# Performance work log

Hardware: AMD Instinct MI355X
Metric: run time of the kernel (lower is better)

The kernel has to match this reference:

```python
import jax, jax.numpy as jnp
import numpy as np

N, SEQ, HID, ENC, E = 16384, 512, 1024, 256, 8


def setup_inputs() -> dict:
    key = jax.random.key(0)
    ks = jax.random.split(key, 8)
    def w(k, shape, fan_in):
        return jax.random.normal(k, shape, dtype=jnp.float32) * (1.0 / np.sqrt(fan_in))
    return {
        "x": jax.random.normal(ks[0], (N, SEQ), dtype=jnp.float32),
        "ids": jax.random.randint(ks[1], (N,), 0, E),
        "W1": w(ks[2], (SEQ, HID), SEQ),
        "b1": jnp.zeros((HID,), jnp.float32),
        "W2": w(ks[3], (HID, ENC), HID),
        "b2": jnp.zeros((ENC,), jnp.float32),
        "W3": w(ks[4], (E, ENC, HID), ENC),
        "b3": jnp.zeros((E, HID), jnp.float32),
        "W4": w(ks[5], (E, HID, SEQ), HID),
        "b4": jnp.zeros((E, SEQ), jnp.float32),
    }


def reference(x, ids, W1, b1, W2, b2, W3, b3, W4, b4):
    # fixed trunk (shared across all combination IDs)
    h = jax.nn.relu(x @ W1 + b1)          # [N, HID]
    z = jax.nn.relu(h @ W2 + b2)          # [N, ENC]
    # per-combination expert head: Linear(enc,hid)+ReLU+Linear(hid,seq)
    n_experts = W3.shape[0]
    oh = jax.nn.one_hot(ids, n_experts, dtype=x.dtype)  # [N, E] row->expert mask
    y = jnp.zeros((x.shape[0], W4.shape[-1]), dtype=x.dtype)
    for e in range(n_experts):  # small fixed expert count; each iter is a big GEMM
        u = jax.nn.relu(z @ W3[e] + b3[e])             # [N, HID]
        y = y + (u @ W4[e] + b4[e]) * oh[:, e:e + 1]   # scatter-back via mask
    return y
```

## Files before the change

kernel.cpp:

```cpp
#include <hip/hip_runtime.h>
#include <hip/hip_bf16.h>

#define NROWS 16384
#define SEQD  512
#define HIDD  1024
#define ENCD  256
#define NEXP  8
#define NBLK  64
#define MAXTILES 136
#define MPAD_MAX (MAXTILES * 128)

using bf16 = __hip_bfloat16;
typedef __bf16 bf16x8 __attribute__((ext_vector_type(8)));
typedef float  f32x4  __attribute__((ext_vector_type(4)));

enum : size_t {
  OFF_XB   = 0,
  OFF_W1T  = OFF_XB  + (size_t)NROWS * SEQD * 2,
  OFF_W2T  = OFF_W1T + (size_t)HIDD * SEQD * 2,
  OFF_H    = OFF_W2T + (size_t)ENCD * HIDD * 2,
  OFF_W3T  = OFF_H   + (size_t)NROWS * HIDD * 2,
  OFF_W4T  = OFF_W3T + (size_t)NEXP * HIDD * ENCD * 2,
  OFF_Z    = OFF_W4T + (size_t)NEXP * SEQD * HIDD * 2,
  OFF_PERM = OFF_Z   + (size_t)NROWS * ENCD * 2,
  OFF_META = OFF_PERM + (size_t)MPAD_MAX * 4,
  OFF_U    = 0,
  WS_NEED  = OFF_META + 8192
};

__device__ __forceinline__ void gload_lds16(const void* g, void* l) {
  __builtin_amdgcn_global_load_lds(
      (const __attribute__((address_space(1))) void*)g,
      (__attribute__((address_space(3))) void*)l, 16, 0, 0);
}

__global__ void prep_k(const float* __restrict__ x,
                       const float* __restrict__ W1, const float* __restrict__ W2,
                       const float* __restrict__ W3, const float* __restrict__ W4,
                       bf16* __restrict__ Xb, bf16* __restrict__ W1t,
                       bf16* __restrict__ W2t, bf16* __restrict__ W3t,
                       bf16* __restrict__ W4t) {
  __shared__ float t[32][33];
  int b = blockIdx.x;
  const int tid = threadIdx.x;
  if (b < 4096) {
    size_t i = (size_t)b * 256 + tid;
    float4 a = ((const float4*)x)[i * 2];
    float4 c = ((const float4*)x)[i * 2 + 1];
    __align__(16) bf16 v[8] = {
      __float2bfloat16(a.x), __float2bfloat16(a.y), __float2bfloat16(a.z), __float2bfloat16(a.w),
      __float2bfloat16(c.x), __float2bfloat16(c.y), __float2bfloat16(c.z), __float2bfloat16(c.w)};
    *(int4*)(Xb + i * 8) = *(const int4*)v;
    return;
  }
  b -= 4096;
  const float* s; bf16* d; int R, C;
  if (b < 512)              { s = W1; d = W1t; R = SEQD; C = HIDD; }
  else if ((b -= 512) < 256){ s = W2; d = W2t; R = HIDD; C = ENCD; }
  else if ((b -= 256) < 2048){
    int z = b >> 8; b &= 255; s = W3 + (size_t)z * ENCD * HIDD; d = W3t + (size_t)z * ENCD * HIDD;
    R = ENCD; C = HIDD;
  } else {
    b -= 2048; int z = b >> 9; b &= 511;
    s = W4 + (size_t)z * HIDD * SEQD; d = W4t + (size_t)z * HIDD * SEQD;
    R = HIDD; C = SEQD;
  }
  const int nbx = C >> 5;
  const int bx = (b % nbx) * 32, by = (b / nbx) * 32;
  const int tx = tid & 31, ty = tid >> 5;
  #pragma unroll
  for (int i = 0; i < 32; i += 8) t[ty + i][tx] = s[(size_t)(by + ty + i) * C + bx + tx];
  __syncthreads();
  #pragma unroll
  for (int i = 0; i < 32; i += 8)
    d[(size_t)(bx + ty + i) * R + by + tx] = __float2bfloat16(t[tx][ty + i]);
}


__global__ void count_k(const int* __restrict__ ids, int* __restrict__ gh) {
  __shared__ int c[NEXP];
  const int tid = threadIdx.x;
  if (tid < NEXP) c[tid] = 0;
  __syncthreads();
  atomicAdd(&c[ids[blockIdx.x * 256 + tid]], 1);
  __syncthreads();
  if (tid < NEXP) gh[blockIdx.x * NEXP + tid] = c[tid];
}

__global__ __launch_bounds__(1024) void bases_k(int* __restrict__ meta,
                                                int* __restrict__ perm) {
  int* gh        = meta;
  int* bases     = meta + 512;
  int* blockbase = meta + 528;
  __shared__ int counts[NEXP];
  __shared__ int base_s[NEXP + 1];
  const int tid = threadIdx.x;
  if (tid < NEXP) {
    int s = 0;
    for (int b = 0; b < NBLK; ++b) s += gh[b * NEXP + tid];
    counts[tid] = s;
  }
  __syncthreads();
  if (tid == 0) {
    int t = 0;
    for (int e = 0; e < NEXP; ++e) { base_s[e] = t; t += (counts[e] + 127) & ~127; }
    base_s[NEXP] = t;
  }
  __syncthreads();
  if (tid < NEXP) {
    int run = base_s[tid];
    for (int b = 0; b < NBLK; ++b) { blockbase[b * NEXP + tid] = run; run += gh[b * NEXP + tid]; }
  }
  if (tid == 0)
    for (int e = 0; e <= NEXP; ++e) bases[e] = base_s[e];
  #pragma unroll
  for (int e = 0; e < NEXP; ++e) {
    int lo = base_s[e] + counts[e];
    int i  = lo + tid;
    if (i < base_s[e + 1]) perm[i] = -1;
  }
}

__global__ void scatter_k(const int* __restrict__ ids, const int* __restrict__ blockbase,
                          int* __restrict__ perm) {
  __shared__ int wavehist[4][NEXP];
  const int tid = threadIdx.x, w = tid >> 6, lane = tid & 63;
  const int n = blockIdx.x * 256 + tid;
  const int e = ids[n];
  const unsigned long long lt = (1ull << lane) - 1ull;
  int myrank = 0;
  #pragma unroll
  for (int ee = 0; ee < NEXP; ++ee) {
    unsigned long long bb = __ballot(e == ee);
    if (ee == e) myrank = __popcll(bb & lt);
    if (lane == 0) wavehist[w][ee] = __popcll(bb);
  }
  __syncthreads();
  int pre = 0;
  for (int w2 = 0; w2 < w; ++w2) pre += wavehist[w2][e];
  perm[blockbase[blockIdx.x * NEXP + e] + pre + myrank] = n;
}

template <bool GATHER_A, bool EXPERT, bool RELU, bool SCATTER_F32>
__global__ __launch_bounds__(256, 2) void gemm128(
    const bf16* __restrict__ A, const bf16* __restrict__ Bt,
    const float* __restrict__ bias, void* __restrict__ Out,
    int Ncols, int K, const int* __restrict__ perm, const int* __restrict__ bases) {
  __shared__ char lds[65536];

  const int tid  = threadIdx.x;
  const int wid  = tid >> 6;
  const int lane = tid & 63;
  const int lm = lane & 15, l4 = lane >> 4;
  const int wm = wid >> 1, wn = wid & 1;

  const int tileM = blockIdx.x, tileN = blockIdx.y;
  int expert = 0;
  if (EXPERT) {
    const int total = bases[8];
    if (tileM * 128 >= total) return;
    const int r0 = tileM * 128;
    #pragma unroll
    for (int e = 1; e < NEXP; ++e) expert += (r0 >= bases[e]) ? 1 : 0;
    Bt   += (size_t)expert * Ncols * K;
    bias += expert * Ncols;
  }
  const int row0 = tileM * 128, col0 = tileN * 128;

  const bf16* gA[4];
  const bf16* gB[4];
  #pragma unroll
  for (int i = 0; i < 4; ++i) {
    int flat = (i * 4 + wid) * 1024 + lane * 16;
    int r    = flat >> 7;
    int cb   = (flat & 127) ^ ((r & 7) << 4);
    int arow;
    if (GATHER_A) {
      int p = perm[row0 + r];
      arow = (p < 0) ? 0 : p;
    } else {
      arow = row0 + r;
    }
    gA[i] = A  + (size_t)arow * K + (cb >> 1);
    gB[i] = Bt + (size_t)(col0 + r) * K + (cb >> 1);
  }

  f32x4 acc[4][4];
  #pragma unroll
  for (int i = 0; i < 4; ++i)
    #pragma unroll
    for (int j = 0; j < 4; ++j) { f32x4 z = {0.f, 0.f, 0.f, 0.f}; acc[i][j] = z; }

  int aoff[4], boff[4];
  const int swz = (lm & 7) << 4;
  #pragma unroll
  for (int i = 0; i < 4; ++i) {
    int ar = wm * 64 + i * 16 + lm;
    aoff[i] = ar * 128 + ((l4 * 16) ^ swz);
    int br = wn * 64 + i * 16 + lm;
    boff[i] = br * 128 + ((l4 * 16) ^ swz);
  }

  const int nk = K >> 6;
  const int ldsoff = (wid * 4) * 1024 + (lane & 3) * 16 + ((lane >> 2) << 8);
  asm volatile("s_waitcnt vmcnt(0)" ::: "memory");
  __builtin_amdgcn_sched_barrier(0);

  #pragma unroll
  for (int i = 0; i < 4; ++i) {
    gload_lds16(gA[i], lds + (i * 4 + wid) * 1024);
    gload_lds16(gB[i], lds + 16384 + (i * 4 + wid) * 1024);
  }
  #pragma unroll
  for (int i = 0; i < 4; ++i) {
    gload_lds16(gA[i] + 64, lds + 32768 + (i * 4 + wid) * 1024);
    gload_lds16(gB[i] + 64, lds + 32768 + 16384 + (i * 4 + wid) * 1024);
  }

  for (int kt = 0; kt < nk; ++kt) {
    if (kt < nk - 1) asm volatile("s_waitcnt vmcnt(8)" ::: "memory");
    else             asm volatile("s_waitcnt vmcnt(0)" ::: "memory");
    asm volatile("s_barrier" ::: "memory");
    __builtin_amdgcn_sched_barrier(0);

    const char* Ac = lds + (kt & 1) * 32768;
    const char* Bc = Ac + 16384;
    #pragma unroll
    for (int kk = 0; kk < 2; ++kk) {
      bf16x8 af[4], bfr[4];
      #pragma unroll
      for (int i = 0; i < 4; ++i) af[i]  = *(const bf16x8*)(Ac + (aoff[i] ^ (kk * 64)));
      #pragma unroll
      for (int i = 0; i < 4; ++i) bfr[i] = *(const bf16x8*)(Bc + (boff[i] ^ (kk * 64)));
      #pragma unroll
      for (int mi = 0; mi < 4; ++mi)
        #pragma unroll
        for (int ni = 0; ni < 4; ++ni)
          acc[mi][ni] = __builtin_amdgcn_mfma_f32_16x16x32_bf16(af[mi], bfr[ni], acc[mi][ni], 0, 0, 0);
    }

    asm volatile("s_barrier" ::: "memory");
    __builtin_amdgcn_sched_barrier(0);
    if (kt + 2 < nk) {
      char* An = lds + (kt & 1) * 32768;
      #pragma unroll
      for (int i = 0; i < 4; ++i) {
        gload_lds16(gA[i] + (size_t)(kt + 2) * 64, An + (i * 4 + wid) * 1024);
        gload_lds16(gB[i] + (size_t)(kt + 2) * 64, An + 16384 + (i * 4 + wid) * 1024);
      }
    }
  }
  (void)ldsoff;

  float bv[4];
  #pragma unroll
  for (int ni = 0; ni < 4; ++ni) bv[ni] = bias[col0 + wn * 64 + ni * 16 + lm];
  #pragma unroll
  for (int mi = 0; mi < 4; ++mi) {
    #pragma unroll
    for (int r = 0; r < 4; ++r) {
      int rowp = row0 + wm * 64 + mi * 16 + l4 * 4 + r;
      int orow = rowp;
      bool valid = true;
      if (SCATTER_F32) {
        int p = perm[rowp];
        valid = (p >= 0);
        orow  = valid ? p : 0;
      }
      #pragma unroll
      for (int ni = 0; ni < 4; ++ni) {
        float v = acc[mi][ni][r] + bv[ni];
        if (RELU) v = v > 0.f ? v : 0.f;
        int n = col0 + wn * 64 + ni * 16 + lm;
        if (SCATTER_F32) {
          if (valid) ((float*)Out)[(size_t)orow * Ncols + n] = v;
        } else {
          ((bf16*)Out)[(size_t)rowp * Ncols + n] = __float2bfloat16(v);
        }
      }
    }
  }
}

extern "C" void kernel_launch(void* const* d_in, const int* in_sizes, int n_in,
                              void* d_out, int out_size, void* d_ws, size_t ws_size,
                              hipStream_t stream) {
  const float* x  = (const float*)d_in[0];
  const int*   ids= (const int*)d_in[1];
  const float* W1 = (const float*)d_in[2];
  const float* b1 = (const float*)d_in[3];
  const float* W2 = (const float*)d_in[4];
  const float* b2 = (const float*)d_in[5];
  const float* W3 = (const float*)d_in[6];
  const float* b3 = (const float*)d_in[7];
  const float* W4 = (const float*)d_in[8];
  const float* b4 = (const float*)d_in[9];

  char* ws = (char*)d_ws;
  bf16* Xb  = (bf16*)(ws + OFF_XB);
  bf16* W1t = (bf16*)(ws + OFF_W1T);
  bf16* W2t = (bf16*)(ws + OFF_W2T);
  bf16* W3t = (bf16*)(ws + OFF_W3T);
  bf16* W4t = (bf16*)(ws + OFF_W4T);
  bf16* H   = (bf16*)(ws + OFF_H);
  bf16* Z   = (bf16*)(ws + OFF_Z);
  bf16* U   = (bf16*)(ws + OFF_U);
  int*  perm      = (int*)(ws + OFF_PERM);
  int*  meta      = (int*)(ws + OFF_META);
  int*  gh        = meta;
  int*  bases     = meta + 512;
  int*  blockbase = meta + 528;

  prep_k<<<dim3(11008), dim3(256), 0, stream>>>(x, W1, W2, W3, W4, Xb, W1t, W2t, W3t, W4t);
  count_k  <<<dim3(NBLK), dim3(256), 0, stream>>>(ids, gh);
  bases_k  <<<dim3(1),    dim3(1024), 0, stream>>>(meta, perm);
  scatter_k<<<dim3(NBLK), dim3(256), 0, stream>>>(ids, blockbase, perm);

  gemm128<false, false, true, false><<<dim3(NROWS / 128, HIDD / 128), dim3(256), 0, stream>>>(
      Xb, W1t, b1, H, HIDD, SEQD, nullptr, nullptr);
  gemm128<false, false, true, false><<<dim3(NROWS / 128, ENCD / 128), dim3(256), 0, stream>>>(
      H, W2t, b2, Z, ENCD, HIDD, nullptr, nullptr);
  gemm128<true, true, true, false><<<dim3(MAXTILES, HIDD / 128), dim3(256), 0, stream>>>(
      Z, W3t, b3, U, HIDD, ENCD, perm, bases);
  gemm128<false, true, false, true><<<dim3(MAXTILES, SEQD / 128), dim3(256), 0, stream>>>(
      U, W4t, b4, d_out, SEQD, HIDD, perm, bases);

  (void)in_sizes; (void)n_in; (void)out_size; (void)ws_size;
}
```

Baseline: 119.4 us.

## Add 256x256 8-wave GEMM for first layer and triple-buffer second GEMM

Adds a new 256x256-tile, 512-thread GEMM kernel for the X@W1 layer. It uses 128KB of double-buffered LDS, interleaves fragment reads with MFMA groups under setprio, and places barriers between the phases. The aim is higher arithmetic intensity per LDS byte and fewer tile loads for the largest trunk GEMM. The existing 128-tile GEMM is generalized to an NSLOTS-deep LDS ring, and the narrow H@W2 GEMM (K=1024, only 2 column tiles) uses 3 slots to hide global latency. The 3-slot variant drops to 1 block per CU because of its 96KB of LDS, so occupancy falls in exchange for deeper prefetch.

```diff
diff --git a/kernel.cpp b/kernel.cpp
--- a/kernel.cpp
+++ b/kernel.cpp
@@ -141,12 +141,12 @@
   perm[blockbase[blockIdx.x * NEXP + e] + pre + myrank] = n;
 }
 
-template <bool GATHER_A, bool EXPERT, bool RELU, bool SCATTER_F32>
-__global__ __launch_bounds__(256, 2) void gemm128(
+template <bool GATHER_A, bool EXPERT, bool RELU, bool SCATTER_F32, int NSLOTS>
+__global__ __launch_bounds__(256, (NSLOTS == 2 ? 2 : 1)) void gemm128(
     const bf16* __restrict__ A, const bf16* __restrict__ Bt,
     const float* __restrict__ bias, void* __restrict__ Out,
     int Ncols, int K, const int* __restrict__ perm, const int* __restrict__ bases) {
-  __shared__ char lds[65536];
+  __shared__ char lds[NSLOTS * 32768];
 
   const int tid  = threadIdx.x;
   const int wid  = tid >> 6;
@@ -202,28 +202,31 @@
   }
 
   const int nk = K >> 6;
-  const int ldsoff = (wid * 4) * 1024 + (lane & 3) * 16 + ((lane >> 2) << 8);
   asm volatile("s_waitcnt vmcnt(0)" ::: "memory");
   __builtin_amdgcn_sched_barrier(0);
 
   #pragma unroll
-  for (int i = 0; i < 4; ++i) {
-    gload_lds16(gA[i], lds + (i * 4 + wid) * 1024);
-    gload_lds16(gB[i], lds + 16384 + (i * 4 + wid) * 1024);
-  }
-  #pragma unroll
-  for (int i = 0; i < 4; ++i) {
-    gload_lds16(gA[i] + 64, lds + 32768 + (i * 4 + wid) * 1024);
-    gload_lds16(gB[i] + 64, lds + 32768 + 16384 + (i * 4 + wid) * 1024);
-  }
-
+  for (int s = 0; s < NSLOTS; ++s) {
+    if (s < nk) {
+      #pragma unroll
+      for (int i = 0; i < 4; ++i) {
+        gload_lds16(gA[i] + (size_t)s * 64, lds + s * 32768 + (i * 4 + wid) * 1024);
+        gload_lds16(gB[i] + (size_t)s * 64, lds + s * 32768 + 16384 + (i * 4 + wid) * 1024);
+      }
+    }
+  }
+
+  int slot = 0;
   for (int kt = 0; kt < nk; ++kt) {
-    if (kt < nk - 1) asm volatile("s_waitcnt vmcnt(8)" ::: "memory");
-    else             asm volatile("s_waitcnt vmcnt(0)" ::: "memory");
+    int inflight = nk - 1 - kt;
+    if (inflight > NSLOTS - 1) inflight = NSLOTS - 1;
+    if (inflight >= 2)      asm volatile("s_waitcnt vmcnt(16)" ::: "memory");
+    else if (inflight == 1) asm volatile("s_waitcnt vmcnt(8)"  ::: "memory");
+    else                    asm volatile("s_waitcnt vmcnt(0)"  ::: "memory");
     asm volatile("s_barrier" ::: "memory");
     __builtin_amdgcn_sched_barrier(0);
 
-    const char* Ac = lds + (kt & 1) * 32768;
+    const char* Ac = lds + slot * 32768;
     const char* Bc = Ac + 16384;
     #pragma unroll
     for (int kk = 0; kk < 2; ++kk) {
@@ -241,16 +244,16 @@
 
     asm volatile("s_barrier" ::: "memory");
     __builtin_amdgcn_sched_barrier(0);
-    if (kt + 2 < nk) {
-      char* An = lds + (kt & 1) * 32768;
+    if (kt + NSLOTS < nk) {
+      char* An = lds + slot * 32768;
       #pragma unroll
       for (int i = 0; i < 4; ++i) {
-        gload_lds16(gA[i] + (size_t)(kt + 2) * 64, An + (i * 4 + wid) * 1024);
-        gload_lds16(gB[i] + (size_t)(kt + 2) * 64, An + 16384 + (i * 4 + wid) * 1024);
-      }
-    }
-  }
-  (void)ldsoff;
+        gload_lds16(gA[i] + (size_t)(kt + NSLOTS) * 64, An + (i * 4 + wid) * 1024);
+        gload_lds16(gB[i] + (size_t)(kt + NSLOTS) * 64, An + 16384 + (i * 4 + wid) * 1024);
+      }
+    }
+    slot = (slot + 1 == NSLOTS) ? 0 : slot + 1;
+  }
 
   float bv[4];
   #pragma unroll
@@ -277,6 +280,162 @@
         } else {
           ((bf16*)Out)[(size_t)rowp * Ncols + n] = __float2bfloat16(v);
         }
+      }
+    }
+  }
+}
+
+__global__ __launch_bounds__(512, 2) void gemm256p(
+    const bf16* __restrict__ A, const bf16* __restrict__ Bt,
+    const float* __restrict__ bias, bf16* __restrict__ Out, int Ncols, int K) {
+  __shared__ char lds[131072];
+
+  const int tid  = threadIdx.x;
+  const int wid  = tid >> 6;
+  const int lane = tid & 63;
+  const int lm = lane & 15, l4 = lane >> 4;
+  const int wm = wid >> 2, wn = wid & 3;
+  const int row0 = blockIdx.x * 256, col0 = blockIdx.y * 256;
+
+  const bf16* gA[4];
+  const bf16* gB[4];
+  #pragma unroll
+  for (int i = 0; i < 4; ++i) {
+    const int flat = i * 8192 + tid * 16;
+    const int r    = flat >> 7;
+    const int cb   = (flat & 127) ^ ((r & 7) << 4);
+    gA[i] = A  + (size_t)(row0 + r) * K + (cb >> 1);
+    gB[i] = Bt + (size_t)(col0 + r) * K + (cb >> 1);
+  }
+
+  f32x4 acc[8][4];
+  #pragma unroll
+  for (int i = 0; i < 8; ++i)
+    #pragma unroll
+    for (int j = 0; j < 4; ++j) { f32x4 z = {0.f, 0.f, 0.f, 0.f}; acc[i][j] = z; }
+
+  int aoff[2][4], boff[2][2];
+  #pragma unroll
+  for (int h = 0; h < 2; ++h)
+    #pragma unroll
+    for (int q = 0; q < 4; ++q) {
+      int row = wm * 128 + h * 64 + q * 16 + lm;
+      aoff[h][q] = row * 128 + ((l4 * 16) ^ ((row & 7) << 4));
+    }
+  #pragma unroll
+  for (int nh = 0; nh < 2; ++nh)
+    #pragma unroll
+    for (int p = 0; p < 2; ++p) {
+      int row = wn * 64 + nh * 32 + p * 16 + lm;
+      boff[nh][p] = row * 128 + ((l4 * 16) ^ ((row & 7) << 4));
+    }
+
+  const int nk = K >> 6;
+  asm volatile("s_waitcnt vmcnt(0)" ::: "memory");
+  __builtin_amdgcn_sched_barrier(0);
+
+  #pragma unroll
+  for (int i = 0; i < 4; ++i) {
+    gload_lds16(gA[i], lds + i * 8192 + tid * 16);
+    gload_lds16(gB[i], lds + 32768 + i * 8192 + tid * 16);
+  }
+  #pragma unroll
+  for (int i = 0; i < 4; ++i) {
+    gload_lds16(gA[i] + 64, lds + 65536 + i * 8192 + tid * 16);
+    gload_lds16(gB[i] + 64, lds + 65536 + 32768 + i * 8192 + tid * 16);
+  }
+  asm volatile("s_waitcnt vmcnt(8)" ::: "memory");
+  asm volatile("s_barrier" ::: "memory");
+  __builtin_amdgcn_sched_barrier(0);
+
+  bf16x8 a[4][2], b[2][2];
+  #pragma unroll
+  for (int q = 0; q < 4; ++q)
+    #pragma unroll
+    for (int kk = 0; kk < 2; ++kk) a[q][kk] = *(const bf16x8*)(lds + (aoff[0][q] ^ (kk * 64)));
+  #pragma unroll
+  for (int p = 0; p < 2; ++p)
+    #pragma unroll
+    for (int kk = 0; kk < 2; ++kk) b[p][kk] = *(const bf16x8*)(lds + 32768 + (boff[0][p] ^ (kk * 64)));
+
+#define MFMA16(MOFF, NOFF)                                                      \
+  __builtin_amdgcn_s_setprio(1);                                                \
+  _Pragma("unroll")                                                             \
+  for (int kk = 0; kk < 2; ++kk)                                                \
+    _Pragma("unroll")                                                           \
+    for (int mf = 0; mf < 4; ++mf)                                              \
+      _Pragma("unroll")                                                         \
+      for (int nf = 0; nf < 2; ++nf)                                            \
+        acc[MOFF + mf][NOFF + nf] = __builtin_amdgcn_mfma_f32_16x16x32_bf16(    \
+            a[mf][kk], b[nf][kk], acc[MOFF + mf][NOFF + nf], 0, 0, 0);          \
+  __builtin_amdgcn_s_setprio(0);
+
+#define RD_A(H, BUFA)                                                           \
+  _Pragma("unroll")                                                             \
+  for (int q = 0; q < 4; ++q)                                                   \
+    _Pragma("unroll")                                                           \
+    for (int kk = 0; kk < 2; ++kk)                                              \
+      a[q][kk] = *(const bf16x8*)((BUFA) + (aoff[H][q] ^ (kk * 64)));
+#define RD_B(NH, BUFB)                                                          \
+  _Pragma("unroll")                                                             \
+  for (int p = 0; p < 2; ++p)                                                   \
+    _Pragma("unroll")                                                           \
+    for (int kk = 0; kk < 2; ++kk)                                              \
+      b[p][kk] = *(const bf16x8*)((BUFB) + (boff[NH][p] ^ (kk * 64)));
+
+  for (int kt = 0; kt < nk; ++kt) {
+    const char* bufA = lds + (kt & 1) * 65536;
+    const char* bufB = bufA + 32768;
+    asm volatile("s_barrier" ::: "memory");
+    MFMA16(0, 0)
+    RD_B(1, bufB)
+    asm volatile("s_barrier" ::: "memory");
+    MFMA16(0, 2)
+    RD_A(1, bufA)
+    asm volatile("s_barrier" ::: "memory");
+    MFMA16(4, 2)
+    RD_B(0, bufB)
+    asm volatile("s_barrier" ::: "memory");
+    MFMA16(4, 0)
+    if (kt + 1 < nk) {
+      asm volatile("s_waitcnt lgkmcnt(0)" ::: "memory");
+      asm volatile("s_barrier" ::: "memory");
+      __builtin_amdgcn_sched_barrier(0);
+      if (kt + 2 < nk) {
+        char* sA = lds + (kt & 1) * 65536;
+        #pragma unroll
+        for (int i = 0; i < 4; ++i) {
+          gload_lds16(gA[i] + (size_t)(kt + 2) * 64, sA + i * 8192 + tid * 16);
+          gload_lds16(gB[i] + (size_t)(kt + 2) * 64, sA + 32768 + i * 8192 + tid * 16);
+        }
+        asm volatile("s_waitcnt vmcnt(8)" ::: "memory");
+      } else {
+        asm volatile("s_waitcnt vmcnt(0)" ::: "memory");
+      }
+      __builtin_amdgcn_sched_barrier(0);
+      const char* nA = lds + ((kt + 1) & 1) * 65536;
+      const char* nB = nA + 32768;
+      RD_A(0, nA)
+      RD_B(0, nB)
+    }
+  }
+#undef MFMA16
+#undef RD_A
+#undef RD_B
+
+  float bv[4];
+  #pragma unroll
+  for (int nf = 0; nf < 4; ++nf) bv[nf] = bias[col0 + wn * 64 + nf * 16 + lm];
+  #pragma unroll
+  for (int mf = 0; mf < 8; ++mf) {
+    #pragma unroll
+    for (int rr = 0; rr < 4; ++rr) {
+      const int rowp = row0 + wm * 128 + mf * 16 + l4 * 4 + rr;
+      #pragma unroll
+      for (int nf = 0; nf < 4; ++nf) {
+        float v = acc[mf][nf][rr] + bv[nf];
+        v = v > 0.f ? v : 0.f;
+        Out[(size_t)rowp * Ncols + col0 + wn * 64 + nf * 16 + lm] = __float2bfloat16(v);
       }
     }
   }
@@ -316,13 +475,13 @@
   bases_k  <<<dim3(1),    dim3(1024), 0, stream>>>(meta, perm);
   scatter_k<<<dim3(NBLK), dim3(256), 0, stream>>>(ids, blockbase, perm);
 
-  gemm128<false, false, true, false><<<dim3(NROWS / 128, HIDD / 128), dim3(256), 0, stream>>>(
-      Xb, W1t, b1, H, HIDD, SEQD, nullptr, nullptr);
-  gemm128<false, false, true, false><<<dim3(NROWS / 128, ENCD / 128), dim3(256), 0, stream>>>(
+  gemm256p<<<dim3(NROWS / 256, HIDD / 256), dim3(512), 0, stream>>>(
+      Xb, W1t, b1, H, HIDD, SEQD);
+  gemm128<false, false, true, false, 3><<<dim3(NROWS / 128, ENCD / 128), dim3(256), 0, stream>>>(
       H, W2t, b2, Z, ENCD, HIDD, nullptr, nullptr);
-  gemm128<true, true, true, false><<<dim3(MAXTILES, HIDD / 128), dim3(256), 0, stream>>>(
+  gemm128<true, true, true, false, 2><<<dim3(MAXTILES, HIDD / 128), dim3(256), 0, stream>>>(
       Z, W3t, b3, U, HIDD, ENCD, perm, bases);
-  gemm128<false, true, false, true><<<dim3(MAXTILES, SEQD / 128), dim3(256), 0, stream>>>(
+  gemm128<false, true, false, true, 2><<<dim3(MAXTILES, SEQD / 128), dim3(256), 0, stream>>>(
       U, W4t, b4, d_out, SEQD, HIDD, perm, bases);
 
   (void)in_sizes; (void)n_in; (void)out_size; (void)ws_size;
```

New measurement: 118.6 us. About the same (-0.7%).

## Fuse x fp32-to-bf16 conversion into first GEMM and merge count into prep

Applied to the files above, without the earlier changes.

Drops the standalone pass that converts x to bf16 and adds a gemm128x variant that loads fp32 x from global memory, converts it in registers and writes it to swizzled LDS, while B still uses direct global-to-LDS loads. The per-block id histogram kernel is folded into the tail blocks of the weight-prep kernel, which removes one launch. This avoids writing and re-reading a 16 MB bf16 copy of x. The cost is a first GEMM that now reads fp32 A eight times over (once per column tile) through register staging, which raises memory traffic and register pressure in that GEMM.

```diff
diff --git a/kernel.cpp b/kernel.cpp
--- a/kernel.cpp
+++ b/kernel.cpp
@@ -34,26 +34,24 @@
       (__attribute__((address_space(3))) void*)l, 16, 0, 0);
 }
 
-__global__ void prep_k(const float* __restrict__ x,
-                       const float* __restrict__ W1, const float* __restrict__ W2,
+__global__ void prep_k(const float* __restrict__ W1, const float* __restrict__ W2,
                        const float* __restrict__ W3, const float* __restrict__ W4,
-                       bf16* __restrict__ Xb, bf16* __restrict__ W1t,
-                       bf16* __restrict__ W2t, bf16* __restrict__ W3t,
-                       bf16* __restrict__ W4t) {
+                       const int* __restrict__ ids,
+                       bf16* __restrict__ W1t, bf16* __restrict__ W2t,
+                       bf16* __restrict__ W3t, bf16* __restrict__ W4t,
+                       int* __restrict__ gh) {
   __shared__ float t[32][33];
   int b = blockIdx.x;
   const int tid = threadIdx.x;
-  if (b < 4096) {
-    size_t i = (size_t)b * 256 + tid;
-    float4 a = ((const float4*)x)[i * 2];
-    float4 c = ((const float4*)x)[i * 2 + 1];
-    __align__(16) bf16 v[8] = {
-      __float2bfloat16(a.x), __float2bfloat16(a.y), __float2bfloat16(a.z), __float2bfloat16(a.w),
-      __float2bfloat16(c.x), __float2bfloat16(c.y), __float2bfloat16(c.z), __float2bfloat16(c.w)};
-    *(int4*)(Xb + i * 8) = *(const int4*)v;
+  if (b >= 6912) {
+    __shared__ int c[NEXP];
+    if (tid < NEXP) c[tid] = 0;
+    __syncthreads();
+    atomicAdd(&c[ids[(b - 6912) * 256 + tid]], 1);
+    __syncthreads();
+    if (tid < NEXP) gh[(b - 6912) * NEXP + tid] = c[tid];
     return;
   }
-  b -= 4096;
   const float* s; bf16* d; int R, C;
   if (b < 512)              { s = W1; d = W1t; R = SEQD; C = HIDD; }
   else if ((b -= 512) < 256){ s = W2; d = W2t; R = HIDD; C = ENCD; }
@@ -76,16 +74,6 @@
     d[(size_t)(bx + ty + i) * R + by + tx] = __float2bfloat16(t[tx][ty + i]);
 }
 
-
-__global__ void count_k(const int* __restrict__ ids, int* __restrict__ gh) {
-  __shared__ int c[NEXP];
-  const int tid = threadIdx.x;
-  if (tid < NEXP) c[tid] = 0;
-  __syncthreads();
-  atomicAdd(&c[ids[blockIdx.x * 256 + tid]], 1);
-  __syncthreads();
-  if (tid < NEXP) gh[blockIdx.x * NEXP + tid] = c[tid];
-}
 
 __global__ __launch_bounds__(1024) void bases_k(int* __restrict__ meta,
                                                 int* __restrict__ perm) {
@@ -202,7 +190,6 @@
   }
 
   const int nk = K >> 6;
-  const int ldsoff = (wid * 4) * 1024 + (lane & 3) * 16 + ((lane >> 2) << 8);
   asm volatile("s_waitcnt vmcnt(0)" ::: "memory");
   __builtin_amdgcn_sched_barrier(0);
 
@@ -250,7 +237,6 @@
       }
     }
   }
-  (void)ldsoff;
 
   float bv[4];
   #pragma unroll
@@ -277,6 +263,137 @@
         } else {
           ((bf16*)Out)[(size_t)rowp * Ncols + n] = __float2bfloat16(v);
         }
+      }
+    }
+  }
+}
+
+__global__ __launch_bounds__(256, 2) void gemm128x(
+    const float* __restrict__ A, const bf16* __restrict__ Bt,
+    const float* __restrict__ bias, bf16* __restrict__ Out, int Ncols, int K) {
+  __shared__ char lds[65536];
+
+  const int tid  = threadIdx.x;
+  const int wid  = tid >> 6;
+  const int lane = tid & 63;
+  const int lm = lane & 15, l4 = lane >> 4;
+  const int wm = wid >> 1, wn = wid & 1;
+  const int row0 = blockIdx.x * 128, col0 = blockIdx.y * 128;
+
+  const int ar_ = tid >> 1, ah = tid & 1;
+  const float* gAx = A + (size_t)(row0 + ar_) * K + ah * 32;
+  int awr[4];
+  #pragma unroll
+  for (int j = 0; j < 4; ++j)
+    awr[j] = ar_ * 128 + ((ah * 64 + j * 16) ^ ((ar_ & 7) << 4));
+
+  const bf16* gB[4];
+  #pragma unroll
+  for (int i = 0; i < 4; ++i) {
+    int flat = (i * 4 + wid) * 1024 + lane * 16;
+    int r    = flat >> 7;
+    int cb   = (flat & 127) ^ ((r & 7) << 4);
+    gB[i] = Bt + (size_t)(col0 + r) * K + (cb >> 1);
+  }
+
+  f32x4 acc[4][4];
+  #pragma unroll
+  for (int i = 0; i < 4; ++i)
+    #pragma unroll
+    for (int j = 0; j < 4; ++j) { f32x4 z = {0.f, 0.f, 0.f, 0.f}; acc[i][j] = z; }
+
+  int aoff[4], boff[4];
+  const int swz = (lm & 7) << 4;
+  #pragma unroll
+  for (int i = 0; i < 4; ++i) {
+    int ar = wm * 64 + i * 16 + lm;
+    aoff[i] = ar * 128 + ((l4 * 16) ^ swz);
+    int br = wn * 64 + i * 16 + lm;
+    boff[i] = br * 128 + ((l4 * 16) ^ swz);
+  }
+
+#define LOAD_A(KT)                                                              \
+  _Pragma("unroll")                                                             \
+  for (int j = 0; j < 8; ++j) av[j] = *(const float4*)(gAx + (KT) * 64 + j * 4);
+#define WRITE_A(SLOTPTR)                                                        \
+  _Pragma("unroll")                                                             \
+  for (int j = 0; j < 4; ++j) {                                                 \
+    __align__(16) bf16 tb[8] = {                                                \
+      __float2bfloat16(av[2*j].x),   __float2bfloat16(av[2*j].y),               \
+      __float2bfloat16(av[2*j].z),   __float2bfloat16(av[2*j].w),               \
+      __float2bfloat16(av[2*j+1].x), __float2bfloat16(av[2*j+1].y),             \
+      __float2bfloat16(av[2*j+1].z), __float2bfloat16(av[2*j+1].w)};            \
+    *(int4*)((SLOTPTR) + awr[j]) = *(const int4*)tb;                            \
+  }
+
+  const int nk = K >> 6;
+  float4 av[8];
+  asm volatile("s_waitcnt vmcnt(0)" ::: "memory");
+  __builtin_amdgcn_sched_barrier(0);
+
+  LOAD_A(0)
+  #pragma unroll
+  for (int i = 0; i < 4; ++i) gload_lds16(gB[i], lds + 16384 + (i * 4 + wid) * 1024);
+  WRITE_A(lds)
+  LOAD_A(1)
+  #pragma unroll
+  for (int i = 0; i < 4; ++i) gload_lds16(gB[i] + 64, lds + 32768 + 16384 + (i * 4 + wid) * 1024);
+  WRITE_A(lds + 32768)
+  asm volatile("s_waitcnt lgkmcnt(0)" ::: "memory");
+  __builtin_amdgcn_sched_barrier(0);
+
+  for (int kt = 0; kt < nk; ++kt) {
+    if (kt + 2 < nk) { LOAD_A(kt + 2) }
+    if (kt + 2 < nk)      asm volatile("s_waitcnt vmcnt(12)" ::: "memory");
+    else if (kt + 1 < nk) asm volatile("s_waitcnt vmcnt(4)"  ::: "memory");
+    else                  asm volatile("s_waitcnt vmcnt(0)"  ::: "memory");
+    asm volatile("s_barrier" ::: "memory");
+    __builtin_amdgcn_sched_barrier(0);
+
+    const char* Ac = lds + (kt & 1) * 32768;
+    const char* Bc = Ac + 16384;
+    #pragma unroll
+    for (int kk = 0; kk < 2; ++kk) {
+      bf16x8 af[4], bfr[4];
+      #pragma unroll
+      for (int i = 0; i < 4; ++i) af[i]  = *(const bf16x8*)(Ac + (aoff[i] ^ (kk * 64)));
+      #pragma unroll
+      for (int i = 0; i < 4; ++i) bfr[i] = *(const bf16x8*)(Bc + (boff[i] ^ (kk * 64)));
+      #pragma unroll
+      for (int mi = 0; mi < 4; ++mi)
+        #pragma unroll
+        for (int ni = 0; ni < 4; ++ni)
+          acc[mi][ni] = __builtin_amdgcn_mfma_f32_16x16x32_bf16(af[mi], bfr[ni], acc[mi][ni], 0, 0, 0);
+    }
+
+    asm volatile("s_barrier" ::: "memory");
+    __builtin_amdgcn_sched_barrier(0);
+    if (kt + 2 < nk) {
+      char* An = lds + (kt & 1) * 32768;
+      #pragma unroll
+      for (int i = 0; i < 4; ++i)
+        gload_lds16(gB[i] + (size_t)(kt + 2) * 64, An + 16384 + (i * 4 + wid) * 1024);
+      WRITE_A(An)
+      asm volatile("s_waitcnt lgkmcnt(0)" ::: "memory");
+      __builtin_amdgcn_sched_barrier(0);
+    }
+  }
+#undef LOAD_A
+#undef WRITE_A
+
+  float bv[4];
+  #pragma unroll
+  for (int ni = 0; ni < 4; ++ni) bv[ni] = bias[col0 + wn * 64 + ni * 16 + lm];
+  #pragma unroll
+  for (int mi = 0; mi < 4; ++mi) {
+    #pragma unroll
+    for (int r = 0; r < 4; ++r) {
+      int rowp = row0 + wm * 64 + mi * 16 + l4 * 4 + r;
+      #pragma unroll
+      for (int ni = 0; ni < 4; ++ni) {
+        float v = acc[mi][ni][r] + bv[ni];
+        v = v > 0.f ? v : 0.f;
+        Out[(size_t)rowp * Ncols + col0 + wn * 64 + ni * 16 + lm] = __float2bfloat16(v);
       }
     }
   }
@@ -297,7 +414,6 @@
   const float* b4 = (const float*)d_in[9];
 
   char* ws = (char*)d_ws;
-  bf16* Xb  = (bf16*)(ws + OFF_XB);
   bf16* W1t = (bf16*)(ws + OFF_W1T);
   bf16* W2t = (bf16*)(ws + OFF_W2T);
   bf16* W3t = (bf16*)(ws + OFF_W3T);
@@ -311,13 +427,12 @@
   int*  bases     = meta + 512;
   int*  blockbase = meta + 528;
 
-  prep_k<<<dim3(11008), dim3(256), 0, stream>>>(x, W1, W2, W3, W4, Xb, W1t, W2t, W3t, W4t);
-  count_k  <<<dim3(NBLK), dim3(256), 0, stream>>>(ids, gh);
+  prep_k<<<dim3(6976), dim3(256), 0, stream>>>(W1, W2, W3, W4, ids, W1t, W2t, W3t, W4t, gh);
   bases_k  <<<dim3(1),    dim3(1024), 0, stream>>>(meta, perm);
   scatter_k<<<dim3(NBLK), dim3(256), 0, stream>>>(ids, blockbase, perm);
 
-  gemm128<false, false, true, false><<<dim3(NROWS / 128, HIDD / 128), dim3(256), 0, stream>>>(
-      Xb, W1t, b1, H, HIDD, SEQD, nullptr, nullptr);
+  gemm128x<<<dim3(NROWS / 128, HIDD / 128), dim3(256), 0, stream>>>(
+      x, W1t, b1, H, HIDD, SEQD);
   gemm128<false, false, true, false><<<dim3(NROWS / 128, ENCD / 128), dim3(256), 0, stream>>>(
       H, W2t, b2, Z, ENCD, HIDD, nullptr, nullptr);
   gemm128<true, true, true, false><<<dim3(MAXTILES, HIDD / 128), dim3(256), 0, stream>>>(
```

Result: slower. 135.9 us (+13.9%).
